# Kernel optimization log

Hardware: AMD Instinct MI355X
Metric: run time of the kernel (lower is better)

Reference implementation:

```python
import jax, jax.numpy as jnp
import numpy as np

B, S, C = 2, 2048, 1536
HQ, HKV = 16, 4
DQK, DV = 128, 96
MAX_POS = 2048
CLIP = 5.0
EPS = 1e-5


def layer_norm(x, g, b):
    mu = jnp.mean(x, axis=-1, keepdims=True)
    var = jnp.mean(jnp.square(x - mu), axis=-1, keepdims=True)
    return (x - mu) * jax.lax.rsqrt(var + EPS) * g + b


def rms_bn(x, g, ms):
    # eval-mode EMA RMS batch-norm: per-channel running mean-square `ms`
    return x * jax.lax.rsqrt(ms + EPS) * g


def rope(x):
    # x: [B, S, H, C] with C even
    c = x.shape[-1]
    nf = c // 2
    s = x.shape[1]
    positions = jnp.arange(s, dtype=x.dtype)
    lin = jnp.arange(nf, dtype=x.dtype)
    end = max(MAX_POS - nf + 1.0, 1.0)
    geom = jnp.exp(jnp.linspace(0.0, jnp.log(jnp.asarray(end, dtype=x.dtype)), nf))
    inv_freq = 1.0 / (lin + geom)
    theta = positions[:, None] * inv_freq          # [S, nf]
    theta = jnp.repeat(theta, 2, axis=-1)[:, None, :]  # [S, 1, C]
    x_rot = jnp.stack([-x[..., 1::2], x[..., ::2]], axis=-1).reshape(x.shape)
    return x * jnp.cos(theta) + x_rot * jnp.sin(theta)


def setup_inputs() -> dict:
    key = jax.random.key(0)
    ks = jax.random.split(key, 8)
    d = {
        'x': jax.random.normal(ks[0], (B, S, C), dtype=jnp.float32),
        'bn1_g': jnp.ones((C,), jnp.float32),
        'bn1_ms': jnp.ones((C,), jnp.float32),
        'Wq': jax.random.normal(ks[1], (C, HQ * DQK), jnp.float32) * 0.02,
        'Wk': jax.random.normal(ks[2], (C, HKV * DQK), jnp.float32) * 0.02,
        'Wv': jax.random.normal(ks[3], (C, HKV * DV), jnp.float32) * 0.02,
        'qn_g': jnp.ones((DQK,), jnp.float32), 'qn_b': jnp.zeros((DQK,), jnp.float32),
        'kn_g': jnp.ones((DQK,), jnp.float32), 'kn_b': jnp.zeros((DQK,), jnp.float32),
        'vn_g': jnp.ones((DV,), jnp.float32), 'vn_b': jnp.zeros((DV,), jnp.float32),
        'Wo': jax.random.normal(ks[4], (HQ * DV, C), jnp.float32) * 0.02,
        'bo': jnp.zeros((C,), jnp.float32),
        'bn2_g': jnp.ones((C,), jnp.float32),
        'bn2_ms': jnp.ones((C,), jnp.float32),
    }
    return d


def reference(x, bn1_g, bn1_ms, Wq, Wk, Wv, qn_g, qn_b, kn_g, kn_b, vn_g, vn_b, Wo, bo, bn2_g, bn2_ms):
    rep = HQ // HKV
    h = rms_bn(x, bn1_g, bn1_ms)                       # [B,S,C]
    q = (h @ Wq).reshape(B, S, HQ, DQK)
    k = (h @ Wk).reshape(B, S, HKV, DQK)
    v = (h @ Wv).reshape(B, S, HKV, DV)
    q = layer_norm(q, qn_g, qn_b)
    k = layer_norm(k, kn_g, kn_b)
    v = layer_norm(v, vn_g, vn_b)
    q = rope(q)
    k = rope(k)
    # torch .repeat(1,1,rep,1) tiles head axis: [h0..hkv-1] * rep
    k = jnp.tile(k, (1, 1, rep, 1))                    # [B,S,HQ,DQK]
    v = jnp.tile(v, (1, 1, rep, 1))                    # [B,S,HQ,DV]
    logits = jnp.einsum('bshc,bShc->bhsS', q, k) / (DQK ** 0.5)
    logits = jnp.tanh(logits / CLIP) * CLIP
    attn = jax.nn.softmax(logits, axis=-1)
    y = jnp.einsum('bhsS,bShc->bshc', attn, v)         # [B,S,HQ,DV]
    y = y.reshape(B, S, HQ * DV)
    y = y @ Wo + bo
    y = rms_bn(y, bn2_g, bn2_ms)
    return y
```

## Files before the change

### kernel.cpp

```cpp
#include <hip/hip_runtime.h>
#include <hip/hip_bf16.h>
#include <math.h>

typedef __hip_bfloat16 bf16;
typedef __attribute__((ext_vector_type(8))) short short8;
typedef __attribute__((ext_vector_type(4))) short short4s;
typedef __attribute__((ext_vector_type(4))) float f32x4;

constexpr int Bb=2, Ss=2048, Cc=1536, HQn=16, HKVn=4, Dqk=128, Dv=96;
constexpr int NR   = Bb*Ss;
constexpr int NQKV = HQn*Dqk + HKVn*Dqk + HKVn*Dv;
constexpr int COL_K = HQn*Dqk;
constexpr int COL_V = COL_K + HKVn*Dqk;
constexpr int NY   = HQn*Dv;
constexpr float EPSf=1e-5f, CLIPf=5.0f;
constexpr float LOG2E = 1.44269504089f;

__device__ __forceinline__ float s2f(short s) {
    unsigned u = ((unsigned)(unsigned short)s) << 16;
    return __builtin_bit_cast(float, u);
}
__device__ __forceinline__ short f2s(float v) {
    bf16 b = __float2bfloat16(v);
    return __builtin_bit_cast(short, b);
}
__device__ __forceinline__ bool is_bf(const void* tagp) {
    return ((*(const unsigned*)tagp) & 0xFFFFu) != 0u;
}
__device__ __forceinline__ float ldd(const void* p, size_t i, bool bf) {
    return bf ? s2f(((const short*)p)[i]) : ((const float*)p)[i];
}
__device__ __forceinline__ void gll16(const void* src, void* lds) {
    __builtin_amdgcn_global_load_lds(
        (const __attribute__((address_space(1))) void*)src,
        (__attribute__((address_space(3))) void*)lds, 16, 0, 0);
}

__global__ __launch_bounds__(256) void k_pre(const void* g1, const void* ms1,
        const void* bo, const void* g2, const void* ms2,
        float* __restrict__ ascale, float* __restrict__ ebias,
        float* __restrict__ escale, float2* __restrict__ tab) {
    bool bf = is_bf(ms1);
    int idx = blockIdx.x*256 + threadIdx.x;
    if (idx < Cc) {
        ascale[idx] = rsqrtf(ldd(ms1,idx,bf) + EPSf) * ldd(g1,idx,bf);
        ebias[idx]  = ldd(bo,idx,bf);
        escale[idx] = rsqrtf(ldd(ms2,idx,bf) + EPSf) * ldd(g2,idx,bf);
    }
    if (idx < Ss*64) {
        int s = idx >> 6, f = idx & 63;
        float geom = expf((float)f * (logf(1985.0f) * (1.0f/63.0f)));
        float invf = 1.0f / ((float)f + geom);
        float th = (float)s * invf;
        tab[idx] = make_float2(cosf(th), sinf(th));
    }
}

__global__ __launch_bounds__(256) void k_bn1(const void* __restrict__ x,
        const float* __restrict__ ascale, short* __restrict__ h, const void* tagp) {
    bool bf = is_bf(tagp);
    size_t i8 = (size_t)(blockIdx.x*256 + threadIdx.x) * 8;
    if (i8 >= (size_t)NR*Cc) return;
    int c = (int)(i8 % Cc);
    float xv[8];
    if (bf) {
        short8 xa = *(const short8*)((const short*)x + i8);
        #pragma unroll
        for (int j=0;j<8;++j) xv[j] = s2f(xa[j]);
    } else {
        const float* xf = (const float*)x + i8;
        #pragma unroll
        for (int j=0;j<8;++j) xv[j] = xf[j];
    }
    short8 o;
    #pragma unroll
    for (int j=0;j<8;++j) o[j] = f2s(xv[j] * ascale[c+j]);
    *(short8*)(h + i8) = o;
}

__global__ __launch_bounds__(256) void k_trw(const void* __restrict__ Wq,
        const void* __restrict__ Wk, const void* __restrict__ Wv,
        const void* __restrict__ Wo, short* __restrict__ WT, const void* tagp) {
    __shared__ short tile[32][33];
    bool bf = is_bf(tagp);
    int gt = blockIdx.x*32;
    int k0 = blockIdx.y*32;
    const void* W; int N, nl;
    if      (gt < 2048) { W = Wq; N = 2048; nl = gt; }
    else if (gt < 2560) { W = Wk; N = 512;  nl = gt - 2048; }
    else if (gt < 2944) { W = Wv; N = 384;  nl = gt - 2560; }
    else                { W = Wo; N = 1536; nl = gt - 2944; }
    int t = threadIdx.x, c = t & 31;
    #pragma unroll
    for (int r8=0; r8<32; r8+=8) {
        int r = r8 + (t>>5);
        tile[r][c] = f2s(ldd(W, (size_t)(k0+r)*N + nl + c, bf));
    }
    __syncthreads();
    #pragma unroll
    for (int r8=0; r8<32; r8+=8) {
        int r = r8 + (t>>5);
        WT[(size_t)(gt + r)*Cc + k0 + c] = tile[c][r];
    }
}

__global__ __launch_bounds__(256) void k_gemm(const short* __restrict__ A,
        const short* __restrict__ BT, void* __restrict__ Cout,
        int M, int N, int K,
        const float* __restrict__ ebias, const float* __restrict__ escale,
        int epi, const void* tagp) {
    __shared__ short As[128*32];
    __shared__ short Bs[128*32];
    const int t = threadIdx.x;
    const int w = t >> 6, lane = t & 63;
    const int l15 = lane & 15, quad = lane >> 4;
    const int wm = (w>>1)*64, wn = (w&1)*64;
    const int m0 = blockIdx.y*128, n0 = blockIdx.x*128;
    const int c0 = lane >> 2;
    const int koff = (lane & 3) * 8;

    f32x4 acc[4][4];
    #pragma unroll
    for (int i=0;i<4;++i)
        #pragma unroll
        for (int j=0;j<4;++j) acc[i][j] = (f32x4){0.f,0.f,0.f,0.f};

    for (int k0 = 0; k0 < K; k0 += 32) {
        __syncthreads();
        #pragma unroll
        for (int c=0; c<2; ++c) {
            int rA = w*32 + c*16;
            const short* ga = A  + (size_t)(m0 + rA + c0)*K + k0 + koff;
            const short* gb = BT + (size_t)(n0 + rA + c0)*K + k0 + koff;
            gll16(ga, &As[rA*32]);
            gll16(gb, &Bs[rA*32]);
        }
        __syncthreads();
        short8 af[4], bfr[4];
        #pragma unroll
        for (int mt=0; mt<4; ++mt)
            af[mt] = *(const short8*)&As[(wm + mt*16 + l15)*32 + quad*8];
        #pragma unroll
        for (int nt=0; nt<4; ++nt)
            bfr[nt] = *(const short8*)&Bs[(wn + nt*16 + l15)*32 + quad*8];
        #pragma unroll
        for (int mt=0; mt<4; ++mt)
            #pragma unroll
            for (int nt=0; nt<4; ++nt)
                acc[mt][nt] = __builtin_amdgcn_mfma_f32_16x16x32_bf16(
                    af[mt], bfr[nt], acc[mt][nt], 0, 0, 0);
    }

    const bool outf32 = epi && !is_bf(tagp);
    #pragma unroll
    for (int mt=0; mt<4; ++mt) {
        #pragma unroll
        for (int nt=0; nt<4; ++nt) {
            int col = n0 + wn + nt*16 + l15;
            float eb = epi ? ebias[col]  : 0.f;
            float es = epi ? escale[col] : 1.f;
            #pragma unroll
            for (int reg=0; reg<4; ++reg) {
                int row = m0 + wm + mt*16 + quad*4 + reg;
                float v = acc[mt][nt][reg];
                if (epi) v = (v + eb) * es;
                if (outf32) ((float*)Cout)[(size_t)row*N + col] = v;
                else        ((short*)Cout)[(size_t)row*N + col] = f2s(v);
            }
        }
    }
}

__global__ __launch_bounds__(256) void k_ln(short* __restrict__ qkvb,
        const float2* __restrict__ tab,
        const void* qg, const void* qb_, const void* kg, const void* kb_,
        const void* vg, const void* vb_, const void* tagp) {
    bool bf = is_bf(tagp);
    int R = blockIdx.x*4 + (threadIdx.x>>6);
    int lane = threadIdx.x & 63;
    int hidx = R % 24, bs = R / 24, s = bs % Ss;
    const void *g, *bia; int coff, D, dorope;
    if (hidx < 16)      { coff = hidx*Dqk;              D = Dqk; g = qg; bia = qb_; dorope = 1; }
    else if (hidx < 20) { coff = COL_K + (hidx-16)*Dqk; D = Dqk; g = kg; bia = kb_; dorope = 1; }
    else                { coff = COL_V + (hidx-20)*Dv;  D = Dv;  g = vg; bia = vb_; dorope = 0; }
    short* p = qkvb + (size_t)bs*NQKV + coff;
    int d0 = lane*2;
    bool act = d0 < D;
    float v0 = 0.f, v1 = 0.f;
    if (act) { v0 = s2f(p[d0]); v1 = s2f(p[d0+1]); }
    float sum = v0 + v1;
    #pragma unroll
    for (int m=1; m<64; m<<=1) sum += __shfl_xor(sum, m);
    float mu = sum / (float)D;
    float c0 = act ? v0-mu : 0.f, c1 = act ? v1-mu : 0.f;
    float sq = c0*c0 + c1*c1;
    #pragma unroll
    for (int m=1; m<64; m<<=1) sq += __shfl_xor(sq, m);
    float r = rsqrtf(sq/(float)D + EPSf);
    if (act) {
        float y0 = c0*r*ldd(g,d0,bf)   + ldd(bia,d0,bf);
        float y1 = c1*r*ldd(g,d0+1,bf) + ldd(bia,d0+1,bf);
        if (dorope) {
            float2 cs = tab[s*64 + lane];
            float t0 = y0*cs.x - y1*cs.y;
            y1 = y1*cs.x + y0*cs.y;
            y0 = t0;
        }
        p[d0] = f2s(y0); p[d0+1] = f2s(y1);
    }
}

__global__ __launch_bounds__(256) void k_trv(const short* __restrict__ qkvb,
        short* __restrict__ vT) {
    __shared__ short tile[32][33];
    int bs0 = blockIdx.x*32;
    int dg0 = blockIdx.y*32;
    int t = threadIdx.x, c = t & 31;
    #pragma unroll
    for (int r8=0; r8<32; r8+=8) {
        int r = r8 + (t>>5);
        tile[r][c] = qkvb[(size_t)(bs0+r)*NQKV + COL_V + dg0 + c];
    }
    __syncthreads();
    int b = bs0 >> 11, s0 = bs0 & 2047;
    int s = s0 + c;
    int sp = (s & ~63) + ((s>>5)&1)*32 + ((s>>2)&3)*8 + ((s>>4)&1)*4 + (s&3);
    #pragma unroll
    for (int r8=0; r8<32; r8+=8) {
        int r = r8 + (t>>5);
        vT[((size_t)(b*384 + dg0 + r))*Ss + sp] = tile[c][r];
    }
}

__global__ __launch_bounds__(512, 4) void k_attn(const short* __restrict__ qkvb,
        const short* __restrict__ vT, short* __restrict__ Yb) {
    __shared__ __align__(16) short smem[2*64*128 + 2*96*64];
    auto Ks  = (short(*)[64*128])smem;
    auto VTs = (short(*)[96*64])(smem + 2*64*128);
    const int wg = blockIdx.x;
    const int xcd = wg & 7, idx = wg >> 3;
    const int b = xcd >> 2, kvh = xcd & 3;
    const int qb = idx >> 2, hsub = idx & 3;
    const int hq = hsub*4 + kvh;
    const int q0 = qb*128;
    const int t = threadIdx.x;
    const int w = t >> 6, lane = t & 63;
    const int qw = w & 3, half = w >> 2;
    const int l15 = lane & 15, quad = lane >> 4;
    const int xr = (l15 & 7) * 16;
    const float ctan = 2.0f * (0.0883883476f / CLIPf) * LOG2E;
    const float c2   = -2.0f * CLIPf * LOG2E;

    const short* Kb = qkvb + ((size_t)b*Ss)*NQKV + COL_K + kvh*Dqk;
    const short* Vb = vT + ((size_t)(b*HKVn + kvh)*Dv)*Ss;

    const int rK = 4*w + (lane>>4);
    const char* kq0 = (const char*)Kb + (size_t)rK*NQKV*2
                    + (((lane&15)*16) ^ ((rK&7)*16));
    const int dv0 = 8*w + (lane>>3);
    const char* vq0 = (const char*)Vb + (size_t)dv0*Ss*2
                    + (((lane&7)*16) ^ ((dv0&7)*16));
    const size_t KADV = (size_t)64*NQKV*2;
    const size_t KOFF2 = (size_t)32*NQKV*2;
    const size_t VOFF2 = (size_t)64*Ss*2;

    auto issue_stage = [&](int pb) {
        char* KD = (char*)&Ks[pb][0];
        char* VD = (char*)&VTs[pb][0];
        gll16(kq0,         KD + w*1024);
        gll16(kq0 + KOFF2, KD + (w+8)*1024);
        gll16(vq0,         VD + w*1024);
        if (w < 4) gll16(vq0 + VOFF2, VD + (w+8)*1024);
        kq0 += KADV; vq0 += 128;
    };

    issue_stage(0);

    short8 qf[2][4];
    #pragma unroll
    for (int qt=0; qt<2; ++qt) {
        const short* qp = qkvb + (size_t)(b*Ss + q0 + qw*32 + qt*16 + l15)*NQKV + hq*Dqk;
        #pragma unroll
        for (int ds=0; ds<4; ++ds) qf[qt][ds] = *(const short8*)(qp + ds*32 + quad*8);
    }

    f32x4 oacc[2][6];
    #pragma unroll
    for (int qt=0; qt<2; ++qt)
        #pragma unroll
        for (int nt=0; nt<6; ++nt) oacc[qt][nt] = (f32x4){0.f,0.f,0.f,0.f};
    float lsum[2] = {0.f, 0.f};

    int p = 0;
    constexpr int NCH = Ss/64;
    for (int kc = 0; kc < NCH; ++kc) {
        __syncthreads();
        if (kc+1 < NCH) issue_stage(p^1);

        const char* KsB  = (const char*)&Ks[p][0];
        const char* VTsB = (const char*)&VTs[p][0];

        short8 pa[2];
        #pragma unroll
        for (int kt=0; kt<2; ++kt) {
            const int r = (half*2 + kt)*16 + l15;
            const char* krow = KsB + r*256;
            short8 kf[4];
            #pragma unroll
            for (int ds=0; ds<4; ++ds)
                kf[ds] = *(const short8*)(krow + ((ds*64 + quad*16) ^ xr));
            f32x4 s0 = (f32x4){0.f,0.f,0.f,0.f}, s1 = (f32x4){0.f,0.f,0.f,0.f};
            __builtin_amdgcn_s_setprio(1);
            #pragma unroll
            for (int ds=0; ds<4; ++ds) {
                s0 = __builtin_amdgcn_mfma_f32_16x16x32_bf16(kf[ds], qf[0][ds], s0, 0, 0, 0);
                s1 = __builtin_amdgcn_mfma_f32_16x16x32_bf16(kf[ds], qf[1][ds], s1, 0, 0, 0);
            }
            __builtin_amdgcn_s_setprio(0);
            #pragma unroll
            for (int j=0; j<4; ++j) {
                float u0 = __builtin_amdgcn_exp2f(s0[j] * ctan);
                float p0 = __builtin_amdgcn_exp2f(c2 * __builtin_amdgcn_rcpf(u0 + 1.0f));
                short ps0 = f2s(p0);
                pa[0][kt*4+j] = ps0; lsum[0] += s2f(ps0);
                float u1 = __builtin_amdgcn_exp2f(s1[j] * ctan);
                float p1 = __builtin_amdgcn_exp2f(c2 * __builtin_amdgcn_rcpf(u1 + 1.0f));
                short ps1 = f2s(p1);
                pa[1][kt*4+j] = ps1; lsum[1] += s2f(ps1);
            }
        }

        __builtin_amdgcn_s_setprio(1);
        #pragma unroll
        for (int nt=0; nt<6; ++nt) {
            const int dvrow = nt*16 + l15;
            short8 vf = *(const short8*)(VTsB + dvrow*128 + ((half*64 + quad*16) ^ xr));
            oacc[0][nt] = __builtin_amdgcn_mfma_f32_16x16x32_bf16(pa[0], vf, oacc[0][nt], 0, 0, 0);
            oacc[1][nt] = __builtin_amdgcn_mfma_f32_16x16x32_bf16(pa[1], vf, oacc[1][nt], 0, 0, 0);
        }
        __builtin_amdgcn_s_setprio(0);
        p ^= 1;
    }

    __syncthreads();
    float* red = (float*)smem;
    const int rbase = (qw*64 + lane)*52;
    if (half == 1) {
        #pragma unroll
        for (int qt=0; qt<2; ++qt)
            #pragma unroll
            for (int nt=0; nt<6; ++nt)
                *(f32x4*)&red[rbase + (qt*6+nt)*4] = oacc[qt][nt];
        red[rbase+48] = lsum[0];
        red[rbase+49] = lsum[1];
    }
    __syncthreads();
    if (half == 0) {
        #pragma unroll
        for (int qt=0; qt<2; ++qt)
            #pragma unroll
            for (int nt=0; nt<6; ++nt) {
                f32x4 o = *(const f32x4*)&red[rbase + (qt*6+nt)*4];
                #pragma unroll
                for (int j=0;j<4;++j) oacc[qt][nt][j] += o[j];
            }
        lsum[0] += red[rbase+48];
        lsum[1] += red[rbase+49];

        float lred[2];
        #pragma unroll
        for (int qt=0; qt<2; ++qt) {
            float l = lsum[qt];
            l += __shfl_xor(l, 16);
            l += __shfl_xor(l, 32);
            lred[qt] = l;
        }
        #pragma unroll
        for (int qt=0; qt<2; ++qt) {
            float rinv[4];
            #pragma unroll
            for (int reg=0; reg<4; ++reg)
                rinv[reg] = __builtin_amdgcn_rcpf(__shfl(lred[qt], quad*4 + reg, 16));
            #pragma unroll
            for (int nt=0; nt<6; ++nt)
                #pragma unroll
                for (int reg=0; reg<4; ++reg) {
                    int row = q0 + qw*32 + qt*16 + quad*4 + reg;
                    Yb[(size_t)(b*Ss + row)*NY + hq*Dv + nt*16 + l15] =
                        f2s(oacc[qt][nt][reg] * rinv[reg]);
                }
        }
    }
}

extern "C" void kernel_launch(void* const* d_in, const int* in_sizes, int n_in,
                              void* d_out, int out_size, void* d_ws, size_t ws_size,
                              hipStream_t stream) {
    const void* x     = d_in[0];
    const void* bn1g  = d_in[1];
    const void* bn1ms = d_in[2];
    const void* Wq    = d_in[3];
    const void* Wk    = d_in[4];
    const void* Wv    = d_in[5];
    const void* qng   = d_in[6];
    const void* qnb   = d_in[7];
    const void* kng   = d_in[8];
    const void* knb   = d_in[9];
    const void* vng   = d_in[10];
    const void* vnb   = d_in[11];
    const void* Wo    = d_in[12];
    const void* bo    = d_in[13];
    const void* bn2g  = d_in[14];
    const void* bn2ms = d_in[15];

    char* wsb = (char*)d_ws;
    float*  ascale = (float*)(wsb);
    float*  ebias  = (float*)(wsb + 6144);
    float*  escale = (float*)(wsb + 12288);
    float2* tab    = (float2*)(wsb + 18432);
    short*  h      = (short*)(wsb + 1067520);
    short*  WT     = (short*)(wsb + 13650432);
    short*  qkv    = (short*)(wsb + 27412992);
    short*  vT     = (short*)(wsb + 51530240);
    short*  y      = (short*)(wsb + 54675968);
    short*  WoT    = WT + (size_t)NQKV*Cc;

    k_pre<<<512, 256, 0, stream>>>(bn1g, bn1ms, bo, bn2g, bn2ms,
                                   ascale, ebias, escale, tab);
    k_bn1<<<(NR*Cc/8 + 255)/256, 256, 0, stream>>>(x, ascale, h, bn1ms);
    k_trw<<<dim3(4480/32, Cc/32), 256, 0, stream>>>(Wq, Wk, Wv, Wo, WT, bn1ms);

    k_gemm<<<dim3(NQKV/128, NR/128), 256, 0, stream>>>(
        h, WT, qkv, NR, NQKV, Cc, nullptr, nullptr, 0, bn1ms);

    k_ln<<<NR*24/4, 256, 0, stream>>>(qkv, tab, qng, qnb, kng, knb, vng, vnb, bn1ms);
    k_trv<<<dim3(NR/32, 384/32), 256, 0, stream>>>(qkv, vT);

    k_attn<<<512, 512, 0, stream>>>(qkv, vT, y);

    k_gemm<<<dim3(Cc/128, NR/128), 256, 0, stream>>>(
        y, WoT, d_out, NR, Cc, NY, ebias, escale, 1, bn1ms);
}
```

Before: 345.6 us.

## Add double-buffered 256x256 QKV GEMM and fold BN1 scale into weights

Replaces the 128x128 QKV projection GEMM with a 512-thread kernel using 256x256 tiles, 64-wide K steps, double-buffered LDS filled by direct global-to-LDS loads, swizzled LDS addressing and a block-index remap for L2 locality. The BN1 per-channel scale is now folded into the transposed Wq/Wk/Wv during weight conversion, so the activation pre-pass becomes a plain bf16 conversion, and it is skipped entirely when the input is already bf16. The attention softmax denominator now accumulates the fp32 probability rather than the rounded bf16 one. The larger tile raises register and LDS pressure, and the padded N of 3072 reads Wo rows as filler columns that are masked on store.

```diff
diff --git a/kernel.cpp b/kernel.cpp
--- a/kernel.cpp
+++ b/kernel.cpp
@@ -57,44 +57,41 @@
 }
 
 __global__ __launch_bounds__(256) void k_bn1(const void* __restrict__ x,
-        const float* __restrict__ ascale, short* __restrict__ h, const void* tagp) {
+        short* __restrict__ h, const void* tagp) {
     bool bf = is_bf(tagp);
     size_t i8 = (size_t)(blockIdx.x*256 + threadIdx.x) * 8;
     if (i8 >= (size_t)NR*Cc) return;
-    int c = (int)(i8 % Cc);
-    float xv[8];
     if (bf) {
-        short8 xa = *(const short8*)((const short*)x + i8);
-        #pragma unroll
-        for (int j=0;j<8;++j) xv[j] = s2f(xa[j]);
+        *(short8*)(h + i8) = *(const short8*)((const short*)x + i8);
     } else {
         const float* xf = (const float*)x + i8;
-        #pragma unroll
-        for (int j=0;j<8;++j) xv[j] = xf[j];
-    }
-    short8 o;
-    #pragma unroll
-    for (int j=0;j<8;++j) o[j] = f2s(xv[j] * ascale[c+j]);
-    *(short8*)(h + i8) = o;
+        short8 o;
+        #pragma unroll
+        for (int j=0;j<8;++j) o[j] = f2s(xf[j]);
+        *(short8*)(h + i8) = o;
+    }
 }
 
 __global__ __launch_bounds__(256) void k_trw(const void* __restrict__ Wq,
         const void* __restrict__ Wk, const void* __restrict__ Wv,
-        const void* __restrict__ Wo, short* __restrict__ WT, const void* tagp) {
+        const void* __restrict__ Wo, short* __restrict__ WT,
+        const float* __restrict__ ascale, const void* tagp) {
     __shared__ short tile[32][33];
     bool bf = is_bf(tagp);
     int gt = blockIdx.x*32;
     int k0 = blockIdx.y*32;
     const void* W; int N, nl;
+    bool doscale = true;
     if      (gt < 2048) { W = Wq; N = 2048; nl = gt; }
     else if (gt < 2560) { W = Wk; N = 512;  nl = gt - 2048; }
     else if (gt < 2944) { W = Wv; N = 384;  nl = gt - 2560; }
-    else                { W = Wo; N = 1536; nl = gt - 2944; }
+    else                { W = Wo; N = 1536; nl = gt - 2944; doscale = false; }
     int t = threadIdx.x, c = t & 31;
     #pragma unroll
     for (int r8=0; r8<32; r8+=8) {
         int r = r8 + (t>>5);
-        tile[r][c] = f2s(ldd(W, (size_t)(k0+r)*N + nl + c, bf));
+        float sc = doscale ? ascale[k0+r] : 1.0f;
+        tile[r][c] = f2s(ldd(W, (size_t)(k0+r)*N + nl + c, bf) * sc);
     }
     __syncthreads();
     #pragma unroll
@@ -166,6 +163,100 @@
                 if (epi) v = (v + eb) * es;
                 if (outf32) ((float*)Cout)[(size_t)row*N + col] = v;
                 else        ((short*)Cout)[(size_t)row*N + col] = f2s(v);
+            }
+        }
+    }
+}
+
+__global__ __launch_bounds__(512, 2) void k_gemm256(const short* __restrict__ A,
+        const short* __restrict__ BT, short* __restrict__ Cout,
+        int M, int Npad, int Nout, int K) {
+    __shared__ __align__(16) short As[2][256*64];
+    __shared__ __align__(16) short Bs[2][256*64];
+    const int t = threadIdx.x;
+    const int w = t >> 6, lane = t & 63;
+    const int wm = w >> 2, wn = w & 3;
+    const int l15 = lane & 15, quad = lane >> 4;
+    const int xr = (l15 & 7) * 16;
+
+    const int nwg = gridDim.x, cpx = nwg >> 3;
+    const int swz = (blockIdx.x & 7)*cpx + (blockIdx.x >> 3);
+    const int ntx = Npad >> 8;
+    const int n0 = (swz % ntx) << 8, m0 = (swz / ntx) << 8;
+
+    const int rA0 = (w*64 + lane) >> 3;
+    const int csw = (((lane & 7) * 16) ^ ((rA0 & 7) << 4));
+    const short* Abase = A  + (size_t)(m0 + rA0)*K;
+    const short* Bbase = BT + (size_t)(n0 + rA0)*K;
+
+    f32x4 acc[8][4];
+    #pragma unroll
+    for (int i=0;i<8;++i)
+        #pragma unroll
+        for (int j=0;j<4;++j) acc[i][j] = (f32x4){0.f,0.f,0.f,0.f};
+
+    auto stage = [&](int kt, int pb) {
+        const char* as = (const char*)Abase + (size_t)kt*128 + csw;
+        const char* bs = (const char*)Bbase + (size_t)kt*128 + csw;
+        char* AD = (char*)&As[pb][0] + w*1024;
+        char* BD = (char*)&Bs[pb][0] + w*1024;
+        const size_t RADV = (size_t)64*K*2;
+        #pragma unroll
+        for (int it=0; it<4; ++it) {
+            gll16(as + it*RADV, AD + it*8192);
+            gll16(bs + it*RADV, BD + it*8192);
+        }
+    };
+
+    stage(0, 0);
+    asm volatile("s_waitcnt vmcnt(0)" ::: "memory");
+    __builtin_amdgcn_s_barrier();
+
+    const int NT = K >> 6;
+    for (int kt = 0; kt < NT; ++kt) {
+        const int cur = kt & 1;
+        const bool pf = (kt+1 < NT);
+        const char* AsB = (const char*)&As[cur][0];
+        const char* BsB = (const char*)&Bs[cur][0];
+        #pragma unroll
+        for (int ph=0; ph<4; ++ph) {
+            if (ph == 0 && pf) stage(kt+1, cur^1);
+            const int mg = ph >> 1, ks = ph & 1;
+            short8 af[4], bf_[4];
+            #pragma unroll
+            for (int i=0; i<4; ++i) {
+                int rowa = wm*128 + (mg*4+i)*16 + l15;
+                af[i] = *(const short8*)(AsB + rowa*128 + ((ks*64 + quad*16) ^ xr));
+                int rowb = wn*64 + i*16 + l15;
+                bf_[i] = *(const short8*)(BsB + rowb*128 + ((ks*64 + quad*16) ^ xr));
+            }
+            __builtin_amdgcn_s_barrier();
+            asm volatile("s_waitcnt lgkmcnt(0)" ::: "memory");
+            __builtin_amdgcn_sched_barrier(0);
+            __builtin_amdgcn_s_setprio(1);
+            #pragma unroll
+            for (int i=0; i<4; ++i)
+                #pragma unroll
+                for (int j=0; j<4; ++j)
+                    acc[mg*4+i][j] = __builtin_amdgcn_mfma_f32_16x16x32_bf16(
+                        af[i], bf_[j], acc[mg*4+i][j], 0, 0, 0);
+            __builtin_amdgcn_s_setprio(0);
+            if (ph == 3 && pf) asm volatile("s_waitcnt vmcnt(0)" ::: "memory");
+            __builtin_amdgcn_s_barrier();
+        }
+    }
+
+    #pragma unroll
+    for (int mt=0; mt<8; ++mt) {
+        #pragma unroll
+        for (int nt=0; nt<4; ++nt) {
+            int col = n0 + wn*64 + nt*16 + l15;
+            if (col < Nout) {
+                #pragma unroll
+                for (int reg=0; reg<4; ++reg) {
+                    int row = m0 + wm*128 + mt*16 + quad*4 + reg;
+                    Cout[(size_t)row*Nout + col] = f2s(acc[mt][nt][reg]);
+                }
             }
         }
     }
@@ -321,12 +412,10 @@
             for (int j=0; j<4; ++j) {
                 float u0 = __builtin_amdgcn_exp2f(s0[j] * ctan);
                 float p0 = __builtin_amdgcn_exp2f(c2 * __builtin_amdgcn_rcpf(u0 + 1.0f));
-                short ps0 = f2s(p0);
-                pa[0][kt*4+j] = ps0; lsum[0] += s2f(ps0);
+                pa[0][kt*4+j] = f2s(p0); lsum[0] += p0;
                 float u1 = __builtin_amdgcn_exp2f(s1[j] * ctan);
                 float p1 = __builtin_amdgcn_exp2f(c2 * __builtin_amdgcn_rcpf(u1 + 1.0f));
-                short ps1 = f2s(p1);
-                pa[1][kt*4+j] = ps1; lsum[1] += s2f(ps1);
+                pa[1][kt*4+j] = f2s(p1); lsum[1] += p1;
             }
         }
 
@@ -427,11 +516,18 @@
 
     k_pre<<<512, 256, 0, stream>>>(bn1g, bn1ms, bo, bn2g, bn2ms,
                                    ascale, ebias, escale, tab);
-    k_bn1<<<(NR*Cc/8 + 255)/256, 256, 0, stream>>>(x, ascale, h, bn1ms);
-    k_trw<<<dim3(4480/32, Cc/32), 256, 0, stream>>>(Wq, Wk, Wv, Wo, WT, bn1ms);
-
-    k_gemm<<<dim3(NQKV/128, NR/128), 256, 0, stream>>>(
-        h, WT, qkv, NR, NQKV, Cc, nullptr, nullptr, 0, bn1ms);
+
+    const short* Agemm;
+    if (in_sizes && in_sizes[0] == (int)((size_t)NR*Cc*2)) {
+        Agemm = (const short*)x;
+    } else {
+        k_bn1<<<(NR*Cc/8 + 255)/256, 256, 0, stream>>>(x, h, bn1ms);
+        Agemm = h;
+    }
+
+    k_trw<<<dim3(4480/32, Cc/32), 256, 0, stream>>>(Wq, Wk, Wv, Wo, WT, ascale, bn1ms);
+
+    k_gemm256<<<dim3(192), 512, 0, stream>>>(Agemm, WT, qkv, NR, 3072, NQKV, Cc);
 
     k_ln<<<NR*24/4, 256, 0, stream>>>(qkv, tab, qng, qnb, kng, knb, vng, vnb, bn1ms);
     k_trv<<<dim3(NR/32, 384/32), 256, 0, stream>>>(qkv, vT);
```

New measurement: 342.5 us. About the same (-0.9%).
